# Kernel optimization log

Hardware: AMD Instinct MI355X
Metric: run time of the kernel (lower is better)

The kernel has to match this reference:

```python
import jax, jax.numpy as jnp
import numpy as np

VOCAB = 32000
HIDDEN = 512


def setup_inputs() -> dict:
    key = jax.random.key(0)
    k1, k2, k3, k4 = jax.random.split(key, 4)
    B, L = 64, 2048  # batch of trees, leaves per (complete binary) tree
    leaf_ids = jax.random.randint(k1, (B, L), 0, VOCAB)
    emb = jax.random.normal(k2, (VOCAB, HIDDEN), dtype=jnp.float32)
    # nn.Linear(2H, H): weight [H, 2H], bias [H]
    lim = 1.0 / np.sqrt(2 * HIDDEN)
    W = jax.random.uniform(k3, (HIDDEN, 2 * HIDDEN), minval=-lim, maxval=lim, dtype=jnp.float32)
    b = jax.random.uniform(k4, (HIDDEN,), minval=-lim, maxval=lim, dtype=jnp.float32)
    return {"leaf_ids": leaf_ids, "emb": emb, "W": W, "b": b}


def reference(leaf_ids, emb, W, b):
    # Preterminal nodes: embed leaf token then activation (matches original order).
    h = jnp.tanh(emb[leaf_ids])  # [B, L, H]
    B, L, H = h.shape
    n_levels = int(np.log2(L))
    # Bottom-up: each internal node concatenates its two children -> linear -> tanh.
    # All same-depth nodes processed as one batched GEMM.
    for _ in range(n_levels):
        n = h.shape[1]
        pairs = h.reshape(B, n // 2, 2 * H)          # concat(left, right) along feature dim
        h = jnp.tanh(jnp.einsum('bnf,hf->bnh', pairs, W) + b)
    return h  # [B, 1, H] root hidden state per tree
```

## Files before the change

### kernel.cpp

```cpp
#include <hip/hip_runtime.h>
#include <stdint.h>

typedef __attribute__((ext_vector_type(8))) short short8;
typedef __attribute__((ext_vector_type(4))) float floatx4;

__device__ __forceinline__ unsigned short f2bf(float x) {
    unsigned int u = __builtin_bit_cast(unsigned int, x);
    unsigned int r = (u + 0x7FFFu + ((u >> 16) & 1u)) >> 16;
    return (unsigned short)r;
}
__device__ __forceinline__ float bf2f(unsigned short x) {
    unsigned int u = ((unsigned int)x) << 16;
    return __builtin_bit_cast(float, u);
}

__device__ __forceinline__ float fast_tanh(float x) {
    float xc = fminf(fmaxf(x, -10.0f), 10.0f);
    float e  = __expf(2.0f * xc);
    float d  = e + 1.0f;
    float r  = __builtin_amdgcn_rcpf(d);
    r = r * (2.0f - d * r);
    return (e - 1.0f) * r;
}

__global__ void wconv(const float4* __restrict__ W4, ushort4* __restrict__ Wb4) {
    int i = blockIdx.x * 256 + threadIdx.x;
    float4 v = W4[i];
    ushort4 o;
    o.x = f2bf(v.x); o.y = f2bf(v.y); o.z = f2bf(v.z); o.w = f2bf(v.w);
    Wb4[i] = o;
}

__global__ void tconv(const float4* __restrict__ emb4, ushort4* __restrict__ embT4) {
    int i = blockIdx.x * 256 + threadIdx.x;
    float4 v = emb4[i];
    ushort4 o;
    o.x = f2bf(fast_tanh(v.x)); o.y = f2bf(fast_tanh(v.y));
    o.z = f2bf(fast_tanh(v.z)); o.w = f2bf(fast_tanh(v.w));
    embT4[i] = o;
}

__global__ void lvl1_add(const int* __restrict__ ids, const ushort* __restrict__ PQ,
                         const float* __restrict__ bias, ushort* __restrict__ h1)
{
    int idx = blockIdx.x * 256 + threadIdx.x;
    int m = idx >> 6;
    int c = (idx & 63) << 3;
    const int il = ids[2 * m], ir = ids[2 * m + 1];
    const short8 p = *reinterpret_cast<const short8*>(PQ + (size_t)il * 512 + c);
    const short8 q = *reinterpret_cast<const short8*>(PQ + 16384000 + (size_t)ir * 512 + c);
    const float4 b0 = *reinterpret_cast<const float4*>(bias + c);
    const float4 b1 = *reinterpret_cast<const float4*>(bias + c + 4);
    short8 o;
    o[0] = (short)f2bf(fast_tanh(bf2f((unsigned short)p[0]) + bf2f((unsigned short)q[0]) + b0.x));
    o[1] = (short)f2bf(fast_tanh(bf2f((unsigned short)p[1]) + bf2f((unsigned short)q[1]) + b0.y));
    o[2] = (short)f2bf(fast_tanh(bf2f((unsigned short)p[2]) + bf2f((unsigned short)q[2]) + b0.z));
    o[3] = (short)f2bf(fast_tanh(bf2f((unsigned short)p[3]) + bf2f((unsigned short)q[3]) + b0.w));
    o[4] = (short)f2bf(fast_tanh(bf2f((unsigned short)p[4]) + bf2f((unsigned short)q[4]) + b1.x));
    o[5] = (short)f2bf(fast_tanh(bf2f((unsigned short)p[5]) + bf2f((unsigned short)q[5]) + b1.y));
    o[6] = (short)f2bf(fast_tanh(bf2f((unsigned short)p[6]) + bf2f((unsigned short)q[6]) + b1.z));
    o[7] = (short)f2bf(fast_tanh(bf2f((unsigned short)p[7]) + bf2f((unsigned short)q[7]) + b1.w));
    *reinterpret_cast<short8*>(h1 + (size_t)idx * 8) = o;
}

#define STG264(buf, k0)                                                         \
    do {                                                                        \
        _Pragma("unroll")                                                       \
        for (int p = 0; p < 4; ++p) {                                           \
            __builtin_amdgcn_global_load_lds(                                   \
                (const __attribute__((address_space(1))) void*)(Ap + (size_t)p * 64 * ASTR + (k0)), \
                (__attribute__((address_space(3))) void*)&sA[buf][p * 4096 + tid * 8], 16, 0, 0); \
            __builtin_amdgcn_global_load_lds(                                   \
                (const __attribute__((address_space(1))) void*)(Bp + (size_t)p * 64 * 1024 + (k0)), \
                (__attribute__((address_space(3))) void*)&sB[buf][p * 4096 + tid * 8], 16, 0, 0); \
        }                                                                       \
    } while (0)

#define CMP264(buf)                                                             \
    do {                                                                        \
        _Pragma("unroll")                                                       \
        for (int ks = 0; ks < 2; ++ks) {                                        \
            const int kq_ = ks * 4 + lh;                                        \
            const int sw_ = ((kq_ ^ (l15 & 7)) << 3);                           \
            short8 a_[8], b_[4];                                                \
            _Pragma("unroll")                                                   \
            for (int ni = 0; ni < 4; ++ni)                                      \
                b_[ni] = *reinterpret_cast<const short8*>(&sB[buf][(rB + ni * 16) * 64 + sw_]); \
            _Pragma("unroll")                                                   \
            for (int mi = 0; mi < 8; ++mi)                                      \
                a_[mi] = *reinterpret_cast<const short8*>(&sA[buf][(rA + mi * 16) * 64 + sw_]); \
            __builtin_amdgcn_s_setprio(1);                                      \
            _Pragma("unroll")                                                   \
            for (int mi = 0; mi < 8; ++mi)                                      \
                _Pragma("unroll")                                               \
                for (int ni = 0; ni < 4; ++ni)                                  \
                    acc[mi][ni] = __builtin_amdgcn_mfma_f32_16x16x32_bf16(      \
                        a_[mi], b_[ni], acc[mi][ni], 0, 0, 0);                  \
            __builtin_amdgcn_s_setprio(0);                                      \
        }                                                                       \
    } while (0)

template<int ASTR, int NT, int MODE>
__global__ __launch_bounds__(512)
void gemm256(const ushort* __restrict__ A, const ushort* __restrict__ Bt,
             const float* __restrict__ bias, ushort* __restrict__ outb)
{
    __shared__ alignas(16) ushort sA[2][16384];
    __shared__ alignas(16) ushort sB[2][16384];

    const int tid  = threadIdx.x;
    const int lane = tid & 63;
    const int w    = tid >> 6;
    const int wr   = w >> 2, wc = w & 3;
    const int l15  = lane & 15;
    const int lh   = lane >> 4;

    int mt, ntile, koff = 0;
    size_t obase = 0;
    if constexpr (MODE == 0) {
        const int nb  = gridDim.x;
        const int per = nb >> 3;
        const int lin = (blockIdx.x & 7) * per + (blockIdx.x >> 3);
        mt = lin >> 1; ntile = lin & 1;
    } else {
        int bid = blockIdx.x;
        const int table = (bid >= 250) ? 1 : 0;
        const int rem = bid - table * 250;
        mt = rem >> 1; ntile = rem & 1;
        koff  = table << 9;
        obase = (size_t)table * 16384000;
    }
    const int m0 = mt * 256, n0 = ntile * 256;

    const int r0 = tid >> 3;
    const int s0 = tid & 7;
    const int swz = ((s0 ^ (r0 & 7)) << 3);
    const ushort* Ap = A  + (size_t)(m0 + r0) * ASTR + swz;
    const ushort* Bp = Bt + (size_t)(n0 + r0) * 1024 + koff + swz;

    const int rA = wr * 128 + l15;
    const int rB = wc * 64  + l15;

    floatx4 acc[8][4] = {};

    STG264(0, 0);
    for (int t = 0; t + 2 < NT; t += 2) {
        asm volatile("s_barrier" ::: "memory");
        STG264(1, (t + 1) * 64);
        asm volatile("s_waitcnt vmcnt(8)" ::: "memory");
        CMP264(0);
        asm volatile("s_barrier" ::: "memory");
        STG264(0, (t + 2) * 64);
        asm volatile("s_waitcnt vmcnt(8)" ::: "memory");
        CMP264(1);
    }
    asm volatile("s_barrier" ::: "memory");
    STG264(1, (NT - 1) * 64);
    asm volatile("s_waitcnt vmcnt(8)" ::: "memory");
    CMP264(0);
    asm volatile("s_barrier" ::: "memory");
    asm volatile("s_waitcnt vmcnt(0)" ::: "memory");
    CMP264(1);

    const int mrow = lh * 4;
    #pragma unroll
    for (int mi = 0; mi < 8; ++mi) {
        #pragma unroll
        for (int ni = 0; ni < 4; ++ni) {
            const int n = n0 + wc * 64 + ni * 16 + l15;
            #pragma unroll
            for (int j = 0; j < 4; ++j) {
                const int m = m0 + wr * 128 + mi * 16 + mrow + j;
                if constexpr (MODE == 0) {
                    float v = fast_tanh(acc[mi][ni][j] + bias[n]);
                    outb[(size_t)m * 512 + n] = f2bf(v);
                } else {
                    outb[obase + (size_t)m * 512 + n] = f2bf(acc[mi][ni][j]);
                }
            }
        }
    }
}

__global__ __launch_bounds__(256)
void small_gemm(const ushort* __restrict__ A, const ushort* __restrict__ Bt,
                const float* __restrict__ bias,
                ushort* __restrict__ outb, float* __restrict__ outf, int last)
{
    __shared__ alignas(16) ushort sA[3][4096];
    __shared__ alignas(16) ushort sB[3][4096];

    const int tid  = threadIdx.x;
    const int lane = tid & 63;
    const int w    = tid >> 6;
    const int l15  = lane & 15;
    const int lh   = lane >> 4;
    const int mt   = blockIdx.x >> 3, nt = blockIdx.x & 7;
    const int m0   = mt * 64, n0 = nt * 64;

    const int r0 = tid >> 3;
    const int s0 = tid & 7;
    const int swz = ((s0 ^ (r0 & 7)) << 3);
    const ushort* Ap = A  + (size_t)(m0 + r0) * 1024 + swz;
    const ushort* Bp = Bt + (size_t)(n0 + r0) * 1024 + swz;

#define STG6(buf, k0)                                                           \
    do {                                                                        \
        __builtin_amdgcn_global_load_lds(                                       \
            (const __attribute__((address_space(1))) void*)(Ap + (k0)),         \
            (__attribute__((address_space(3))) void*)&sA[buf][tid * 8], 16, 0, 0); \
        __builtin_amdgcn_global_load_lds(                                       \
            (const __attribute__((address_space(1))) void*)(Ap + 32 * 1024 + (k0)), \
            (__attribute__((address_space(3))) void*)&sA[buf][2048 + tid * 8], 16, 0, 0); \
        __builtin_amdgcn_global_load_lds(                                       \
            (const __attribute__((address_space(1))) void*)(Bp + (k0)),         \
            (__attribute__((address_space(3))) void*)&sB[buf][tid * 8], 16, 0, 0); \
        __builtin_amdgcn_global_load_lds(                                       \
            (const __attribute__((address_space(1))) void*)(Bp + 32 * 1024 + (k0)), \
            (__attribute__((address_space(3))) void*)&sB[buf][2048 + tid * 8], 16, 0, 0); \
    } while (0)

    const int rb = w * 16 + l15;
    floatx4 acc[4] = {};

#define CMP6(buf)                                                               \
    do {                                                                        \
        _Pragma("unroll")                                                       \
        for (int ks = 0; ks < 2; ++ks) {                                        \
            const int kq = ks * 4 + lh;                                         \
            const short8 b_ = *reinterpret_cast<const short8*>(                 \
                &sB[buf][rb * 64 + ((kq ^ (rb & 7)) << 3)]);                    \
            __builtin_amdgcn_s_setprio(1);                                      \
            _Pragma("unroll")                                                   \
            for (int mi = 0; mi < 4; ++mi) {                                    \
                const int ra = mi * 16 + l15;                                   \
                const short8 a_ = *reinterpret_cast<const short8*>(             \
                    &sA[buf][ra * 64 + ((kq ^ (l15 & 7)) << 3)]);               \
                acc[mi] = __builtin_amdgcn_mfma_f32_16x16x32_bf16(              \
                    a_, b_, acc[mi], 0, 0, 0);                                  \
            }                                                                   \
            __builtin_amdgcn_s_setprio(0);                                      \
        }                                                                       \
    } while (0)

    STG6(0, 0);
    STG6(1, 64);
    for (int t3 = 0; t3 < 12; t3 += 3) {
        asm volatile("s_barrier" ::: "memory");
        STG6(2, (t3 + 2) * 64);
        asm volatile("s_waitcnt vmcnt(4)" ::: "memory");
        CMP6(0);
        asm volatile("s_barrier" ::: "memory");
        STG6(0, (t3 + 3) * 64);
        asm volatile("s_waitcnt vmcnt(4)" ::: "memory");
        CMP6(1);
        asm volatile("s_barrier" ::: "memory");
        STG6(1, (t3 + 4) * 64);
        asm volatile("s_waitcnt vmcnt(4)" ::: "memory");
        CMP6(2);
    }
    asm volatile("s_barrier" ::: "memory");
    STG6(2, 14 * 64);
    asm volatile("s_waitcnt vmcnt(8)" ::: "memory");
    CMP6(0);
    asm volatile("s_barrier" ::: "memory");
    STG6(0, 15 * 64);
    asm volatile("s_waitcnt vmcnt(8)" ::: "memory");
    CMP6(1);
    asm volatile("s_barrier" ::: "memory");
    asm volatile("s_waitcnt vmcnt(4)" ::: "memory");
    CMP6(2);
    asm volatile("s_barrier" ::: "memory");
    asm volatile("s_waitcnt vmcnt(0)" ::: "memory");
    CMP6(0);
#undef CMP6
#undef STG6

    const int n  = n0 + w * 16 + l15;
    const float bb = bias[n];
    #pragma unroll
    for (int mi = 0; mi < 4; ++mi) {
        #pragma unroll
        for (int j = 0; j < 4; ++j) {
            const int m = m0 + mi * 16 + lh * 4 + j;
            float v = fast_tanh(acc[mi][j] + bb);
            if (last) outf[(size_t)m * 512 + n] = v;
            else      outb[(size_t)m * 512 + n] = f2bf(v);
        }
    }
}

extern "C" void kernel_launch(void* const* d_in, const int* in_sizes, int n_in,
                              void* d_out, int out_size, void* d_ws, size_t ws_size,
                              hipStream_t stream) {
    const int*   ids  = (const int*)d_in[0];
    const float* emb  = (const float*)d_in[1];
    const float* W    = (const float*)d_in[2];
    const float* bias = (const float*)d_in[3];
    float* out = (float*)d_out;

    unsigned short* Wb   = (unsigned short*)d_ws;
    unsigned short* embT = Wb + 524288;
    unsigned short* PQ   = embT + 16384000;
    unsigned short* hB   = PQ + 32768000;
    unsigned short* hA   = hB + 33554432;

    wconv<<<512, 256, 0, stream>>>((const float4*)W, (ushort4*)Wb);
    tconv<<<16000, 256, 0, stream>>>((const float4*)emb, (ushort4*)embT);

    gemm256<512, 8, 1><<<500, 512, 0, stream>>>(embT, Wb, bias, PQ);
    lvl1_add<<<16384, 256, 0, stream>>>(ids, PQ, bias, hB);

    int M = 32768;
    for (int l = 2; l <= 4; ++l) {
        const unsigned short* in = (l & 1) ? hA : hB;
        unsigned short*       ob = (l & 1) ? hB : hA;
        gemm256<1024, 16, 0><<<(M / 256) * 2, 512, 0, stream>>>(in, Wb, bias, ob);
        M >>= 1;
    }
    for (int l = 5; l <= 11; ++l) {
        const unsigned short* in = (l & 1) ? hA : hB;
        unsigned short*       ob = (l & 1) ? hB : hA;
        small_gemm<<<(M / 64) * 8, 256, 0, stream>>>(in, Wb, bias, ob, out,
                                                     l == 11 ? 1 : 0);
        M >>= 1;
    }
}
```

Before: 279.7 us.

## Add 128x128-tile level GEMM with LDS direct loads for levels three and four

Introduces a new level_gemm kernel using 128x128 output tiles, 256 threads, a triple-buffered global_load_lds pipeline with swizzled LDS layout, and an XCD-aware block remap. It replaces the 256-row gemm256 launches for tree levels 3 and 4, which have fewer rows and would launch only a few hundred large blocks. The aim is better occupancy and latency hiding on these mid-size levels, at the cost of lower per-block reuse and a hardcoded K loop of 1024.

```diff
diff --git a/kernel.cpp b/kernel.cpp
--- a/kernel.cpp
+++ b/kernel.cpp
@@ -182,6 +182,112 @@
     }
 }
 
+#define STAGE_(buf, k0)                                                         \
+    do {                                                                        \
+        __builtin_amdgcn_global_load_lds(                                       \
+            (const __attribute__((address_space(1))) void*)(Ap + (k0)),         \
+            (__attribute__((address_space(3))) void*)&sA[buf][tid * 8], 16, 0, 0); \
+        __builtin_amdgcn_global_load_lds(                                       \
+            (const __attribute__((address_space(1))) void*)(Ap + 64 * 1024 + (k0)), \
+            (__attribute__((address_space(3))) void*)&sA[buf][2048 + tid * 8], 16, 0, 0); \
+        __builtin_amdgcn_global_load_lds(                                       \
+            (const __attribute__((address_space(1))) void*)(Bp + (k0)),         \
+            (__attribute__((address_space(3))) void*)&sB[buf][tid * 8], 16, 0, 0); \
+        __builtin_amdgcn_global_load_lds(                                       \
+            (const __attribute__((address_space(1))) void*)(Bp + 64 * 1024 + (k0)), \
+            (__attribute__((address_space(3))) void*)&sB[buf][2048 + tid * 8], 16, 0, 0); \
+    } while (0)
+
+#define COMPUTE_(cur)                                                           \
+    do {                                                                        \
+        short8 a_[4], b_[4];                                                    \
+        _Pragma("unroll")                                                       \
+        for (int mi = 0; mi < 4; ++mi)                                          \
+            a_[mi] = *reinterpret_cast<const short8*>(&sA[cur][(rA + mi * 16) * 32 + kksw]); \
+        _Pragma("unroll")                                                       \
+        for (int ni = 0; ni < 4; ++ni)                                          \
+            b_[ni] = *reinterpret_cast<const short8*>(&sB[cur][(rB + ni * 16) * 32 + kksw]); \
+        __builtin_amdgcn_s_setprio(1);                                          \
+        _Pragma("unroll")                                                       \
+        for (int mi = 0; mi < 4; ++mi)                                          \
+            _Pragma("unroll")                                                   \
+            for (int ni = 0; ni < 4; ++ni)                                      \
+                acc[mi][ni] = __builtin_amdgcn_mfma_f32_16x16x32_bf16(          \
+                    a_[mi], b_[ni], acc[mi][ni], 0, 0, 0);                      \
+        __builtin_amdgcn_s_setprio(0);                                          \
+    } while (0)
+
+__global__ __launch_bounds__(256)
+void level_gemm(const ushort* __restrict__ A, const ushort* __restrict__ Bt,
+                const float* __restrict__ bias,
+                ushort* __restrict__ outb, int M)
+{
+    const int nb  = gridDim.x;
+    int bid = blockIdx.x;
+    const int per = nb >> 3;
+    const int lin = (bid & 7) * per + (bid >> 3);
+    const int mt = lin >> 2, nt = lin & 3;
+    const int m0 = mt * 128, n0 = nt * 128;
+
+    __shared__ alignas(16) ushort sA[3][4096];
+    __shared__ alignas(16) ushort sB[3][4096];
+
+    const int tid  = threadIdx.x;
+    const int lane = tid & 63;
+    const int w    = tid >> 6;
+    const int wr   = w >> 1, wc = w & 1;
+
+    const int sr    = tid >> 2;
+    const int swcol = (((tid & 3) ^ ((tid >> 3) & 3)) << 3);
+    const ushort* Ap = A  + (size_t)(m0 + sr) * 1024 + swcol;
+    const ushort* Bp = Bt + (size_t)(n0 + sr) * 1024 + swcol;
+
+    const int rA   = wr * 64 + (lane & 15);
+    const int rB   = wc * 64 + (lane & 15);
+    const int kksw = (((lane >> 4) ^ ((lane >> 1) & 3)) << 3);
+
+    floatx4 acc[4][4] = {};
+
+    STAGE_(0, 0);
+    STAGE_(1, 32);
+    for (int t = 0; t < 30; t += 3) {
+        asm volatile("s_barrier" ::: "memory");
+        STAGE_(2, (t + 2) * 32);
+        asm volatile("s_waitcnt vmcnt(4)" ::: "memory");
+        COMPUTE_(0);
+        asm volatile("s_barrier" ::: "memory");
+        STAGE_(0, (t + 3) * 32);
+        asm volatile("s_waitcnt vmcnt(4)" ::: "memory");
+        COMPUTE_(1);
+        asm volatile("s_barrier" ::: "memory");
+        STAGE_(1, (t + 4) * 32);
+        asm volatile("s_waitcnt vmcnt(4)" ::: "memory");
+        COMPUTE_(2);
+    }
+    asm volatile("s_barrier" ::: "memory");
+    asm volatile("s_waitcnt vmcnt(0)" ::: "memory");
+    COMPUTE_(0);
+    asm volatile("s_barrier" ::: "memory");
+    asm volatile("s_waitcnt vmcnt(0)" ::: "memory");
+    COMPUTE_(1);
+
+    const int mrow = (lane >> 4) * 4;
+    const int ncol = lane & 15;
+    #pragma unroll
+    for (int mi = 0; mi < 4; ++mi)
+        #pragma unroll
+        for (int ni = 0; ni < 4; ++ni) {
+            const int n = n0 + wc * 64 + ni * 16 + ncol;
+            const float bb = bias[n];
+            #pragma unroll
+            for (int j = 0; j < 4; ++j) {
+                const int m = m0 + wr * 64 + mi * 16 + mrow + j;
+                float v = fast_tanh(acc[mi][ni][j] + bb);
+                outb[(size_t)m * 512 + n] = f2bf(v);
+            }
+        }
+}
+
 __global__ __launch_bounds__(256)
 void small_gemm(const ushort* __restrict__ A, const ushort* __restrict__ Bt,
                 const float* __restrict__ bias,
@@ -311,13 +417,12 @@
     gemm256<512, 8, 1><<<500, 512, 0, stream>>>(embT, Wb, bias, PQ);
     lvl1_add<<<16384, 256, 0, stream>>>(ids, PQ, bias, hB);
 
-    int M = 32768;
-    for (int l = 2; l <= 4; ++l) {
-        const unsigned short* in = (l & 1) ? hA : hB;
-        unsigned short*       ob = (l & 1) ? hB : hA;
-        gemm256<1024, 16, 0><<<(M / 256) * 2, 512, 0, stream>>>(in, Wb, bias, ob);
-        M >>= 1;
-    }
+    gemm256<1024, 16, 0><<<256, 512, 0, stream>>>(hB, Wb, bias, hA);
+
+    level_gemm<<<512, 256, 0, stream>>>(hA, Wb, bias, hB, 16384);
+    level_gemm<<<256, 256, 0, stream>>>(hB, Wb, bias, hA, 8192);
+
+    int M = 4096;
     for (int l = 5; l <= 11; ++l) {
         const unsigned short* in = (l & 1) ? hA : hB;
         unsigned short*       ob = (l & 1) ? hB : hA;
```

Result: faster. 260.7 us (-6.8%).
